# Kernel optimization log

Measured on AMD Instinct MI355X. Metric: run time of the kernel, lower is better.

## Reference

```python
import jax, jax.numpy as jnp
import numpy as np

HID = 256  # hardcoded LSTM hidden size in the module


def _lstm_cell(x, h, c, W_ih, W_hh, b_ih, b_hh):
    # PyTorch gate order: i, f, g, o. x,h: [1,HID]; W_*: [4H,HID]; b_*: [4H]
    gates = x @ W_ih.T + h @ W_hh.T + b_ih + b_hh  # [1,4H]
    i, f, g, o = jnp.split(gates, 4, axis=-1)
    c_new = jax.nn.sigmoid(f) * c + jax.nn.sigmoid(i) * jnp.tanh(g)
    h_new = jax.nn.sigmoid(o) * jnp.tanh(c_new)
    return h_new, c_new


def setup_inputs() -> dict:
    key = jax.random.key(0)
    ks = jax.random.split(key, 9)
    s = 0.05
    return {
        "zm_1": jax.random.normal(ks[0], (1, HID), jnp.float32) * s,
        "W_ih": jax.random.normal(ks[1], (4 * HID, HID), jnp.float32) * s,
        "W_hh": jax.random.normal(ks[2], (4 * HID, HID), jnp.float32) * s,
        "b_ih": jax.random.normal(ks[3], (4 * HID,), jnp.float32) * s,
        "b_hh": jax.random.normal(ks[4], (4 * HID,), jnp.float32) * s,
        "W_loc": jax.random.normal(ks[5], (64, HID), jnp.float32) * s,
        "b_loc": jax.random.normal(ks[6], (64,), jnp.float32) * s,
        "W_scale": jax.random.normal(ks[7], (64, HID), jnp.float32) * s,
        "b_scale": jax.random.normal(ks[8], (64,), jnp.float32) * s,
        "K": 7,
        "batch_size": 32768,
    }


def reference(zm_1, W_ih, W_hh, b_ih, b_hh, W_loc, b_loc, W_scale, b_scale, K, batch_size):
    zm_size = W_loc.shape[0]
    h0 = jnp.zeros((1, HID), zm_1.dtype)
    c0 = jnp.zeros((1, HID), zm_1.dtype)

    def step(carry, _):
        x, h, c = carry
        h_new, c_new = _lstm_cell(x, h, c, W_ih, W_hh, b_ih, b_hh)
        # LSTM output z == h_new; it is also the next step's input
        return (h_new, h_new, c_new), h_new

    _, zs = jax.lax.scan(step, (zm_1, h0, c0), None, length=K - 1)  # [K-1,1,HID]
    p_z = jnp.concatenate([zm_1[None], zs], axis=0).reshape(K, HID)  # [K,HID]

    loc = p_z @ W_loc.T + b_loc        # [K,zm]
    scale = p_z @ W_scale.T + b_scale  # [K,zm]
    # repeat over batch dim -> [K*batch_size, zm]
    loc = jnp.broadcast_to(loc[:, None, :], (K, batch_size, zm_size)).reshape(-1, zm_size)
    scale = jnp.broadcast_to(scale[:, None, :], (K, batch_size, zm_size)).reshape(-1, zm_size)
    return loc, scale
```

## Files before the change

kernel.cpp:

```cpp
#include <hip/hip_runtime.h>
#include <cstdint>
#include <cstddef>

#define HID    256
#define NROW   1024
#define KSTEPS 7
#define ZM     64
#define BATCH  32768
#define NCHAIN 64
#define NGRID  512
#define VEC_PER_SEG (BATCH * ZM / 4)
#define VEC_PER_BLK (14 * VEC_PER_SEG / NGRID)

typedef float f32x4 __attribute__((ext_vector_type(4)));

#define WS_GATES 0
#define WS_PZ    (6 * NROW)
#define WS_TAB   (6 * NROW + 6 * HID)
#define WS_FLAG  (6 * NROW + 6 * HID + 896)

#define MAGICS(s) (0x3A9F17C5u + (unsigned)(s) * 0x9E3779B9u)
#define MAGICT    0x7C61B2EDu

__device__ __forceinline__ float sigf(float x)       { return 1.0f / (1.0f + __expf(-x)); }
__device__ __forceinline__ float tanhf_fast(float x) { return 1.0f - 2.0f / (__expf(2.0f * x) + 1.0f); }

__device__ __forceinline__ float dot4(f32x4 a, f32x4 b) {
    return a.x * b.x + a.y * b.y + a.z * b.z + a.w * b.w;
}

__device__ __forceinline__ void st_agent_f(float* p, float v) {
    __hip_atomic_store((unsigned int*)p, __float_as_uint(v),
                       __ATOMIC_RELAXED, __HIP_MEMORY_SCOPE_AGENT);
}
__device__ __forceinline__ float ld_agent_f(const float* p) {
    return __uint_as_float(__hip_atomic_load((const unsigned int*)p,
                       __ATOMIC_RELAXED, __HIP_MEMORY_SCOPE_AGENT));
}
__device__ __forceinline__ void st_agent_u(unsigned* p, unsigned v) {
    __hip_atomic_store(p, v, __ATOMIC_RELAXED, __HIP_MEMORY_SCOPE_AGENT);
}
__device__ __forceinline__ unsigned ld_agent_u(const unsigned* p) {
    return __hip_atomic_load(p, __ATOMIC_RELAXED, __HIP_MEMORY_SCOPE_AGENT);
}

__global__ __launch_bounds__(256, 2) void fused_kernel(
    const float* __restrict__ zm1,
    const float* __restrict__ Wih, const float* __restrict__ Whh,
    const float* __restrict__ bih, const float* __restrict__ bhh,
    const float* __restrict__ Wloc, const float* __restrict__ bloc,
    const float* __restrict__ Wsc,  const float* __restrict__ bsc,
    float* __restrict__ ws, f32x4* __restrict__ out)
{
    const int t = threadIdx.x, b = blockIdx.x;
    __shared__ float hsh[HID];
    __shared__ float psh[HID];
    unsigned* stepflag = (unsigned*)(ws + WS_FLAG);
    unsigned* tabflag  = stepflag + 6 * NCHAIN;

    if (b < NCHAIN) {
        const int row = b * 16 + (t >> 4);
        const int l16 = t & 15;
        const f32x4* wi4 = (const f32x4*)(Wih + (size_t)row * HID + l16 * 16);
        const f32x4* wh4 = (const f32x4*)(Whh + (size_t)row * HID + l16 * 16);
        f32x4 wsum[4];
        #pragma unroll
        for (int kk = 0; kk < 4; ++kk) wsum[kk] = wi4[kk] + wh4[kk];
        const float bihr = bih[row], bhhr = bhh[row];

        {
            const f32x4* x4 = (const f32x4*)(zm1 + l16 * 16);
            float part = 0.f;
            #pragma unroll
            for (int kk = 0; kk < 4; ++kk) part += dot4(wi4[kk], x4[kk]);
            part += __shfl_xor(part, 1);
            part += __shfl_xor(part, 2);
            part += __shfl_xor(part, 4);
            part += __shfl_xor(part, 8);
            if (l16 == 0) st_agent_f(&ws[WS_GATES + row], part + bihr + bhhr);
        }
        if (b == 0) st_agent_f(&ws[WS_PZ + t], zm1[t]);
        __syncthreads();
        if (t == 0) st_agent_u(&stepflag[b], MAGICS(0));

        float c_reg = 0.f;
        #pragma unroll 1
        for (int s = 1; s <= 5; ++s) {
            if (t < NCHAIN)
                while (ld_agent_u(&stepflag[(s - 1) * NCHAIN + t]) != MAGICS(s - 1)) {}
            __syncthreads();
            const float* gp = ws + WS_GATES + (size_t)(s - 1) * NROW;
            float gi = ld_agent_f(gp + t);
            float gf = ld_agent_f(gp + HID + t);
            float gg = ld_agent_f(gp + 2 * HID + t);
            float go = ld_agent_f(gp + 3 * HID + t);
            float cn = sigf(gf) * c_reg + sigf(gi) * tanhf_fast(gg);
            c_reg = cn;
            float h  = sigf(go) * tanhf_fast(cn);
            if (b == 0) st_agent_f(&ws[WS_PZ + (size_t)s * HID + t], h);
            hsh[t] = h;
            __syncthreads();
            float p = 0.f;
            const f32x4* h4 = (const f32x4*)hsh + l16 * 4;
            #pragma unroll
            for (int kk = 0; kk < 4; ++kk) p += dot4(wsum[kk], h4[kk]);
            p += __shfl_xor(p, 1);
            p += __shfl_xor(p, 2);
            p += __shfl_xor(p, 4);
            p += __shfl_xor(p, 8);
            if (l16 == 0) st_agent_f(&ws[WS_GATES + (size_t)s * NROW + row], p + bihr + bhhr);
            __syncthreads();
            if (t == 0) st_agent_u(&stepflag[s * NCHAIN + b], MAGICS(s));
        }

        if (b < 14) {
            if (t < NCHAIN)
                while (ld_agent_u(&stepflag[5 * NCHAIN + t]) != MAGICS(5)) {}
            __syncthreads();
            const int m = b % KSTEPS;
            {
                const float* gp = ws + WS_GATES + (size_t)5 * NROW;
                float gi = ld_agent_f(gp + t);
                float gf = ld_agent_f(gp + HID + t);
                float gg = ld_agent_f(gp + 2 * HID + t);
                float go = ld_agent_f(gp + 3 * HID + t);
                float cn = sigf(gf) * c_reg + sigf(gi) * tanhf_fast(gg);
                hsh[t] = sigf(go) * tanhf_fast(cn);
                if (m < 6) psh[t] = ld_agent_f(&ws[WS_PZ + (size_t)m * HID + t]);
            }
            __syncthreads();
            const int which = b / KSTEPS;
            const int j = t >> 2, q = t & 3;
            const float* W  = which ? Wsc : Wloc;
            const float  bb = which ? bsc[j] : bloc[j];
            const f32x4* w4 = (const f32x4*)(W + (size_t)j * HID);
            const f32x4* p4 = (m == 6) ? (const f32x4*)hsh : (const f32x4*)psh;
            float acc = 0.f;
            #pragma unroll
            for (int kk = 0; kk < 16; ++kk) acc += dot4(w4[q * 16 + kk], p4[q * 16 + kk]);
            acc += __shfl_xor(acc, 1);
            acc += __shfl_xor(acc, 2);
            if (q == 0) st_agent_f(&ws[WS_TAB + b * ZM + j], acc + bb);
            __syncthreads();
            if (t == 0) st_agent_u(&tabflag[b], MAGICT);
        }
    }

    const uint64_t base = (uint64_t)b * VEC_PER_BLK;
    const int wm0 = (int)(base >> 19);
    const int wm1 = (int)((base + VEC_PER_BLK - 1) >> 19);
    if (t == 0)
        while (ld_agent_u(&tabflag[wm0]) != MAGICT) __builtin_amdgcn_s_sleep(2);
    if (t == 1 && wm1 != wm0)
        while (ld_agent_u(&tabflag[wm1]) != MAGICT) __builtin_amdgcn_s_sleep(2);
    __syncthreads();
    const int r4 = (t & 15) * 4;
    f32x4 v0, v1;
    {
        const float* tp = ws + WS_TAB + wm0 * ZM + r4;
        v0.x = ld_agent_f(tp);     v0.y = ld_agent_f(tp + 1);
        v0.z = ld_agent_f(tp + 2); v0.w = ld_agent_f(tp + 3);
    }
    if (wm1 != wm0) {
        const float* tp = ws + WS_TAB + wm1 * ZM + r4;
        v1.x = ld_agent_f(tp);     v1.y = ld_agent_f(tp + 1);
        v1.z = ld_agent_f(tp + 2); v1.w = ld_agent_f(tp + 3);
    } else {
        v1 = v0;
    }
    const int kswitch = (int)(((((uint64_t)(wm0 + 1)) << 19) - base) >> 8);
    #pragma unroll 8
    for (int k = 0; k < VEC_PER_BLK / 256; ++k) {
        f32x4 v = (k < kswitch) ? v0 : v1;
        __builtin_nontemporal_store(v, &out[base + (uint64_t)k * 256 + t]);
    }
}

extern "C" void kernel_launch(void* const* d_in, const int* in_sizes, int n_in,
                              void* d_out, int out_size, void* d_ws, size_t ws_size,
                              hipStream_t stream) {
    const float* zm1  = (const float*)d_in[0];
    const float* Wih  = (const float*)d_in[1];
    const float* Whh  = (const float*)d_in[2];
    const float* bih  = (const float*)d_in[3];
    const float* bhh  = (const float*)d_in[4];
    const float* Wloc = (const float*)d_in[5];
    const float* bloc = (const float*)d_in[6];
    const float* Wsc  = (const float*)d_in[7];
    const float* bsc  = (const float*)d_in[8];
    float* ws = (float*)d_ws;

    fused_kernel<<<NGRID, 256, 0, stream>>>(zm1, Wih, Whh, bih, bhh,
                                            Wloc, bloc, Wsc, bsc,
                                            ws, (f32x4*)d_out);
}
```

Measured before the change: 164.1 us.

## Emit projection tables as soon as each LSTM step finishes; remap output blocks

Each projection block now preloads its W_loc/W_scale row slice into registers and computes its table entry for step m right after step m's hidden state is available, instead of waiting for the full recurrence to end. This removes the staging buffer for intermediate hidden states and lets the output-writing blocks for early steps start broadcasting while the recurrence is still running. Output segments are also remapped so non-chain blocks take the earliest segments and chain blocks take the tail. The trade-off is 64 extra vector registers per thread in chain blocks and extra barriers inside the step loop for the projecting blocks.

```diff
diff --git a/kernel.cpp b/kernel.cpp
--- a/kernel.cpp
+++ b/kernel.cpp
@@ -15,9 +15,8 @@
 typedef float f32x4 __attribute__((ext_vector_type(4)));
 
 #define WS_GATES 0
-#define WS_PZ    (6 * NROW)
-#define WS_TAB   (6 * NROW + 6 * HID)
-#define WS_FLAG  (6 * NROW + 6 * HID + 896)
+#define WS_TAB   (6 * NROW)
+#define WS_FLAG  (6 * NROW + 14 * ZM)
 
 #define MAGICS(s) (0x3A9F17C5u + (unsigned)(s) * 0x9E3779B9u)
 #define MAGICT    0x7C61B2EDu
@@ -53,8 +52,7 @@
     float* __restrict__ ws, f32x4* __restrict__ out)
 {
     const int t = threadIdx.x, b = blockIdx.x;
-    __shared__ float hsh[HID];
-    __shared__ float psh[HID];
+    __shared__ __align__(16) float hsh[HID];
     unsigned* stepflag = (unsigned*)(ws + WS_FLAG);
     unsigned* tabflag  = stepflag + 6 * NCHAIN;
 
@@ -68,6 +66,19 @@
         for (int kk = 0; kk < 4; ++kk) wsum[kk] = wi4[kk] + wh4[kk];
         const float bihr = bih[row], bhhr = bhh[row];
 
+        const int m     = b % KSTEPS;
+        const int which = b / KSTEPS;
+        const int j = t >> 2, q = t & 3;
+        f32x4 wreg[16];
+        float bproj = 0.f;
+        if (b < 14) {
+            const float* W  = which ? Wsc : Wloc;
+            const f32x4* w4 = (const f32x4*)(W + (size_t)j * HID);
+            #pragma unroll
+            for (int kk = 0; kk < 16; ++kk) wreg[kk] = w4[q * 16 + kk];
+            bproj = which ? bsc[j] : bloc[j];
+        }
+
         {
             const f32x4* x4 = (const f32x4*)(zm1 + l16 * 16);
             float part = 0.f;
@@ -79,9 +90,20 @@
             part += __shfl_xor(part, 8);
             if (l16 == 0) st_agent_f(&ws[WS_GATES + row], part + bihr + bhhr);
         }
-        if (b == 0) st_agent_f(&ws[WS_PZ + t], zm1[t]);
         __syncthreads();
         if (t == 0) st_agent_u(&stepflag[b], MAGICS(0));
+
+        if (b < 14 && m == 0) {
+            const f32x4* p4 = (const f32x4*)zm1;
+            float acc = 0.f;
+            #pragma unroll
+            for (int kk = 0; kk < 16; ++kk) acc += dot4(wreg[kk], p4[q * 16 + kk]);
+            acc += __shfl_xor(acc, 1);
+            acc += __shfl_xor(acc, 2);
+            if (q == 0) st_agent_f(&ws[WS_TAB + b * ZM + j], acc + bproj);
+            __syncthreads();
+            if (t == 0) st_agent_u(&tabflag[b], MAGICT);
+        }
 
         float c_reg = 0.f;
         #pragma unroll 1
@@ -97,7 +119,6 @@
             float cn = sigf(gf) * c_reg + sigf(gi) * tanhf_fast(gg);
             c_reg = cn;
             float h  = sigf(go) * tanhf_fast(cn);
-            if (b == 0) st_agent_f(&ws[WS_PZ + (size_t)s * HID + t], h);
             hsh[t] = h;
             __syncthreads();
             float p = 0.f;
@@ -111,42 +132,46 @@
             if (l16 == 0) st_agent_f(&ws[WS_GATES + (size_t)s * NROW + row], p + bihr + bhhr);
             __syncthreads();
             if (t == 0) st_agent_u(&stepflag[s * NCHAIN + b], MAGICS(s));
-        }
-
-        if (b < 14) {
+
+            if (b < 14 && m == s) {
+                const f32x4* p4 = (const f32x4*)hsh;
+                float acc = 0.f;
+                #pragma unroll
+                for (int kk = 0; kk < 16; ++kk) acc += dot4(wreg[kk], p4[q * 16 + kk]);
+                acc += __shfl_xor(acc, 1);
+                acc += __shfl_xor(acc, 2);
+                if (q == 0) st_agent_f(&ws[WS_TAB + b * ZM + j], acc + bproj);
+                __syncthreads();
+                if (t == 0) st_agent_u(&tabflag[b], MAGICT);
+            }
+        }
+
+        if (b < 14 && m == 6) {
             if (t < NCHAIN)
                 while (ld_agent_u(&stepflag[5 * NCHAIN + t]) != MAGICS(5)) {}
             __syncthreads();
-            const int m = b % KSTEPS;
-            {
-                const float* gp = ws + WS_GATES + (size_t)5 * NROW;
-                float gi = ld_agent_f(gp + t);
-                float gf = ld_agent_f(gp + HID + t);
-                float gg = ld_agent_f(gp + 2 * HID + t);
-                float go = ld_agent_f(gp + 3 * HID + t);
-                float cn = sigf(gf) * c_reg + sigf(gi) * tanhf_fast(gg);
-                hsh[t] = sigf(go) * tanhf_fast(cn);
-                if (m < 6) psh[t] = ld_agent_f(&ws[WS_PZ + (size_t)m * HID + t]);
-            }
-            __syncthreads();
-            const int which = b / KSTEPS;
-            const int j = t >> 2, q = t & 3;
-            const float* W  = which ? Wsc : Wloc;
-            const float  bb = which ? bsc[j] : bloc[j];
-            const f32x4* w4 = (const f32x4*)(W + (size_t)j * HID);
-            const f32x4* p4 = (m == 6) ? (const f32x4*)hsh : (const f32x4*)psh;
+            const float* gp = ws + WS_GATES + (size_t)5 * NROW;
+            float gi = ld_agent_f(gp + t);
+            float gf = ld_agent_f(gp + HID + t);
+            float gg = ld_agent_f(gp + 2 * HID + t);
+            float go = ld_agent_f(gp + 3 * HID + t);
+            float cn = sigf(gf) * c_reg + sigf(gi) * tanhf_fast(gg);
+            hsh[t] = sigf(go) * tanhf_fast(cn);
+            __syncthreads();
+            const f32x4* p4 = (const f32x4*)hsh;
             float acc = 0.f;
             #pragma unroll
-            for (int kk = 0; kk < 16; ++kk) acc += dot4(w4[q * 16 + kk], p4[q * 16 + kk]);
+            for (int kk = 0; kk < 16; ++kk) acc += dot4(wreg[kk], p4[q * 16 + kk]);
             acc += __shfl_xor(acc, 1);
             acc += __shfl_xor(acc, 2);
-            if (q == 0) st_agent_f(&ws[WS_TAB + b * ZM + j], acc + bb);
+            if (q == 0) st_agent_f(&ws[WS_TAB + b * ZM + j], acc + bproj);
             __syncthreads();
             if (t == 0) st_agent_u(&tabflag[b], MAGICT);
         }
     }
 
-    const uint64_t base = (uint64_t)b * VEC_PER_BLK;
+    const int bb = (b >= NCHAIN) ? (b - NCHAIN) : (b + (NGRID - NCHAIN));
+    const uint64_t base = (uint64_t)bb * VEC_PER_BLK;
     const int wm0 = (int)(base >> 19);
     const int wm1 = (int)((base + VEC_PER_BLK - 1) >> 19);
     if (t == 0)
```

After: 152.8 us. 1.07x faster.
